# Kernel optimization log

Hardware: AMD Instinct MI355X
Metric: run time of the kernel (lower is better)

The kernel has to match this reference:

```python
import jax, jax.numpy as jnp
import numpy as np
from jax import lax

EPS = 1e-5
B, T, H, L, K = 64, 1024, 12, 120, 5  # batch, seq len, hidden, lstm layers, conv kernel


def _init(key, shape, scale):
    return scale * jax.random.normal(key, shape, dtype=jnp.float32)


def setup_inputs() -> dict:
    key = jax.random.key(0)
    ks = jax.random.split(key, 16)
    return {
        "x": jax.random.normal(ks[0], (B, 6, T), dtype=jnp.float32),
        "conv_acc_w": _init(ks[1], (6, 6, K), 0.3),
        "conv_acc_b": jnp.zeros((6,), jnp.float32),
        "bn1_gamma": jnp.ones((6,), jnp.float32),
        "bn1_beta": jnp.zeros((6,), jnp.float32),
        "conv_ang_w": _init(ks[2], (6, 6, K), 0.3),
        "conv_ang_b": jnp.zeros((6,), jnp.float32),
        "bn2_gamma": jnp.ones((6,), jnp.float32),
        "bn2_beta": jnp.zeros((6,), jnp.float32),
        "attn_w": _init(ks[3], (H, 6), 0.4),
        "attn_b": jnp.zeros((H,), jnp.float32),
        "lstm_wih": _init(ks[4], (L, 4 * H, H), 0.2),
        "lstm_whh": _init(ks[5], (L, 4 * H, H), 0.2),
        "lstm_bih": _init(ks[6], (L, 4 * H), 0.1),
        "lstm_bhh": _init(ks[7], (L, 4 * H), 0.1),
        "lin1_w": _init(ks[8], (H, H), 0.3),
        "lin1_b": jnp.zeros((H,), jnp.float32),
        "lin2_w": _init(ks[9], (H, H), 0.3),
        "lin2_b": jnp.zeros((H,), jnp.float32),
        "mu_w": _init(ks[10], (H, H), 0.3),
        "mu_b": jnp.zeros((H,), jnp.float32),
        "sigma_w": _init(ks[11], (H, H), 0.3),
        "sigma_b": jnp.zeros((H,), jnp.float32),
    }


def _conv1d(x, w, b):
    # x: (B, C, T) valid conv, matches nn.Conv1d
    y = lax.conv_general_dilated(x, w, (1,), "VALID", dimension_numbers=("NCH", "OIH", "NCH"))
    return y + b[None, :, None]


def _batchnorm(x, gamma, beta):
    # training-mode BatchNorm1d: biased batch stats over (N, T)
    mean = jnp.mean(x, axis=(0, 2), keepdims=True)
    var = jnp.var(x, axis=(0, 2), keepdims=True)
    return (x - mean) * lax.rsqrt(var + EPS) * gamma[None, :, None] + beta[None, :, None]


def _lstm_stack(seq_tbh, wih, whh, bias):
    # seq_tbh: (T', B, H); stacked 120-layer LSTM, torch gate order (i, f, g, o)
    b = seq_tbh.shape[1]
    h0 = jnp.zeros((b, H), seq_tbh.dtype)

    def layer(seq, p):
        w_ih, w_hh, bb = p

        def step(carry, xt):
            h, c = carry
            g = xt @ w_ih.T + h @ w_hh.T + bb  # (B, 4H)
            i, f, gg, o = jnp.split(g, 4, axis=-1)
            c_new = jax.nn.sigmoid(f) * c + jax.nn.sigmoid(i) * jnp.tanh(gg)
            h_new = jax.nn.sigmoid(o) * jnp.tanh(c_new)
            return (h_new, c_new), h_new

        (h_T, _), out = lax.scan(step, (h0, h0), seq)
        return out, h_T

    _, h_last = lax.scan(layer, seq_tbh, (wih, whh, bias))
    return h_last  # (L, B, H): final hidden state of every layer


def _forward(x, conv_acc_w, conv_acc_b, bn1_gamma, bn1_beta, conv_ang_w, conv_ang_b,
             bn2_gamma, bn2_beta, attn_w, attn_b, lstm_wih, lstm_whh, lstm_bih, lstm_bhh,
             lin1_w, lin1_b, lin2_w, lin2_b, mu_w, mu_b, sigma_w, sigma_b):
    out_acc = jax.nn.relu(_batchnorm(_conv1d(x, conv_acc_w, conv_acc_b), bn1_gamma, bn1_beta))
    out_ang = jax.nn.relu(_batchnorm(_conv1d(out_acc, conv_ang_w, conv_ang_b), bn2_gamma, bn2_beta))
    feat = jax.nn.relu(jnp.einsum("bct,hc->bth", out_ang, attn_w) + attn_b)  # (B, T-8, H)
    seq = jnp.transpose(feat, (1, 0, 2))  # (T', B, H) time-major for scan
    h_last = _lstm_stack(seq, lstm_wih, lstm_whh, lstm_bih + lstm_bhh)
    h = jnp.transpose(h_last, (1, 0, 2))  # (B, L, H) == hidden_state.permute(1,0,2)
    h = jax.nn.relu(h @ lin1_w.T + lin1_b)
    out = jax.nn.relu(h @ lin2_w.T + lin2_b)
    mu = out @ mu_w.T + mu_b
    log_var = jax.nn.softplus(out @ sigma_w.T + sigma_b)
    return out, mu, log_var


def reference(x, conv_acc_w, conv_acc_b, bn1_gamma, bn1_beta, conv_ang_w, conv_ang_b,
              bn2_gamma, bn2_beta, attn_w, attn_b, lstm_wih, lstm_whh, lstm_bih, lstm_bhh,
              lin1_w, lin1_b, lin2_w, lin2_b, mu_w, mu_b, sigma_w, sigma_b):
    return _forward(x, conv_acc_w, conv_acc_b, bn1_gamma, bn1_beta, conv_ang_w, conv_ang_b,
                    bn2_gamma, bn2_beta, attn_w, attn_b, lstm_wih, lstm_whh, lstm_bih, lstm_bhh,
                    lin1_w, lin1_b, lin2_w, lin2_b, mu_w, mu_b, sigma_w, sigma_b)
```

## Files before the change

kernel.cpp:

```cpp
#include <hip/hip_runtime.h>
#include <math.h>

#define NLAY 120
#define TT   1016
#define NB   64
#define RB   8
#define IRS  32
#define TPB  384
#define BIGF (1 << 20)

typedef float v2f __attribute__((ext_vector_type(2)));

__device__ __forceinline__ float fast_rcp(float x) { return __builtin_amdgcn_rcpf(x); }
__device__ __forceinline__ float fast_sig(float x) { return fast_rcp(1.f + __expf(-x)); }
__device__ __forceinline__ float fast_tanh(float x) { return 1.f - 2.f * fast_rcp(1.f + __expf(2.f * x)); }

__device__ __forceinline__ int poll_ge_ag(const int* p, int tgt, int cur) {
  long g = 0;
  while (cur < tgt) {
    cur = __hip_atomic_load(p, __ATOMIC_RELAXED, __HIP_MEMORY_SCOPE_AGENT);
    if (++g > 2000000L) break;
  }
  return cur;
}
__device__ __forceinline__ int poll_ge_wg(const int* p, int tgt, int cur) {
  long g = 0;
  while (cur < tgt) {
    cur = __hip_atomic_load(p, __ATOMIC_RELAXED, __HIP_MEMORY_SCOPE_WORKGROUP);
    if (++g > 2000000L) break;
  }
  return cur;
}

__global__ void k_conv(const float* __restrict__ xin, const float* __restrict__ cw,
                       const float* __restrict__ cb, const float* __restrict__ aff,
                       float* __restrict__ yout, float* __restrict__ stat,
                       int Tin, int Tout, int use_aff)
{
  const int bx = blockIdx.x;
  const int b = bx / 6, co = bx - b * 6;
  const int tid = threadIdx.x;
  __shared__ float wsh[30];
  __shared__ float ssh[6], shsh[6];
  if (tid < 30) wsh[tid] = cw[co * 30 + tid];
  if (tid < 6) {
    ssh[tid]  = use_aff ? aff[tid] : 1.f;
    shsh[tid] = use_aff ? aff[6 + tid] : 0.f;
  }
  __syncthreads();
  const float bias = cb[co];
  float lsum = 0.f, lsq = 0.f;
  for (int t = tid; t < Tout; t += 256) {
    float acc = bias;
#pragma unroll
    for (int ci = 0; ci < 6; ++ci) {
      const float* xr = xin + ((size_t)b * 6 + ci) * Tin + t;
      const float s = ssh[ci], sh = shsh[ci];
#pragma unroll
      for (int k = 0; k < 5; ++k) {
        float v = xr[k];
        if (use_aff) v = fmaxf(fmaf(s, v, sh), 0.f);
        acc += wsh[ci * 5 + k] * v;
      }
    }
    yout[((size_t)b * 6 + co) * Tout + t] = acc;
    lsum += acc; lsq += acc * acc;
  }
  __shared__ float rs[256], rq[256];
  rs[tid] = lsum; rq[tid] = lsq;
  __syncthreads();
  for (int s = 128; s > 0; s >>= 1) {
    if (tid < s) { rs[tid] += rs[tid + s]; rq[tid] += rq[tid + s]; }
    __syncthreads();
  }
  if (tid == 0) { atomicAdd(&stat[co], rs[0]); atomicAdd(&stat[6 + co], rq[0]); }
}

__global__ void k_finalize(const float* __restrict__ stat,
                           const float* __restrict__ gamma, const float* __restrict__ beta,
                           float* __restrict__ aff, float invN)
{
  const int c = threadIdx.x;
  if (c < 6) {
    float mean = stat[c] * invN;
    float var  = stat[6 + c] * invN - mean * mean;
    float sc   = gamma[c] * rsqrtf(var + 1e-5f);
    aff[c]     = sc;
    aff[6 + c] = fmaf(-mean, sc, beta[c]);
  }
}

__global__ void k_attn(const float* __restrict__ y2, const float* __restrict__ aff2,
                       const float* __restrict__ aw, const float* __restrict__ ab,
                       float* __restrict__ seq0)
{
  const int t = blockIdx.x;
  const int tid = threadIdx.x;
  __shared__ float zb[6 * 64];
  if (tid < 384) {
    const int c = tid >> 6, bb = tid & 63;
    float v = y2[((size_t)bb * 6 + c) * TT + t];
    zb[c * 64 + bb] = fmaxf(fmaf(aff2[c], v, aff2[6 + c]), 0.f);
  }
  __syncthreads();
  const int b = tid / 12, j = tid - b * 12;
  float acc = ab[j];
#pragma unroll
  for (int c = 0; c < 6; ++c) acc += aw[j * 6 + c] * zb[c * 64 + b];
  seq0[(size_t)t * 768 + tid] = fmaxf(acc, 0.f);
}

__global__ __launch_bounds__(TPB, 2) void k_lstm(
    const float* __restrict__ wih, const float* __restrict__ whh,
    const float* __restrict__ bih, const float* __restrict__ bhh,
    const float* __restrict__ seq0, float* __restrict__ ring,
    int* __restrict__ prog, int* __restrict__ cons,
    float* __restrict__ hfin)
{
  const int bid  = blockIdx.x;
  const int c    = bid >> 2;
  const int seg  = bid & 3;
  const int tid  = threadIdx.x;
  const int w    = tid >> 6;
  const int lane = tid & 63;
  const int p    = lane / 12;
  const int j    = lane - p * 12;
  const bool act = (p < 5);
  const int pc   = act ? p : 0;
  const int l    = seg * 30 + w * 5 + pc;

  __shared__ __align__(16) float hloc[6][2][60];
  __shared__ __align__(16) float iring[5][IRS][12];
  __shared__ __align__(16) float xring[2][16][12];
  __shared__ __align__(16) float oring[16][12];
  __shared__ int pflag[6];
  __shared__ int cflag[8];
  float* xrf = &xring[0][0][0];

  if (tid < 6) pflag[tid] = 0;
  if (tid < 8) cflag[tid] = 0;
  if (lane < 60) { hloc[w][0][lane] = 0.f; hloc[w][1][lane] = 0.f; }
  __syncthreads();

  v2f wx_if[12], wx_go[12], wh_if[12], wh_go[12];
  v2f b_if = (v2f){0.f, 0.f}, b_go = (v2f){0.f, 0.f};
  if (act) {
    const float* wi = wih + l * 576;
    const float* wh = whh + l * 576;
#pragma unroll
    for (int k = 0; k < 12; ++k) {
      wx_if[k] = (v2f){ wi[(j     ) * 12 + k], wi[(j + 12) * 12 + k] };
      wx_go[k] = (v2f){ wi[(j + 24) * 12 + k], wi[(j + 36) * 12 + k] };
      wh_if[k] = (v2f){ wh[(j     ) * 12 + k], wh[(j + 12) * 12 + k] };
      wh_go[k] = (v2f){ wh[(j + 24) * 12 + k], wh[(j + 36) * 12 + k] };
    }
    const float* ba = bih + l * 48;
    const float* bb = bhh + l * 48;
    b_if = (v2f){ ba[j]      + bb[j],      ba[j + 12] + bb[j + 12] };
    b_go = (v2f){ ba[j + 24] + bb[j + 24], ba[j + 36] + bb[j + 36] };
  }

  const int hop_in  = c * 3 + seg - 1;
  const int hop_out = c * 3 + seg;
  const float* rin  = ring + (size_t)((seg > 0) ? hop_in : 0) * (RB * 192);
  float*       rout = ring + (size_t)((seg < 3) ? hop_out : 0) * (RB * 192);
  const bool is_feeder = (w == 0);
  const bool is_tailer = (w == 5) && (seg < 3);

  const int f0 = lane, f1 = lane + 64, f2 = lane + 128;
  const int s0o0 = (f0 / 12) * 768 + (f0 % 12);
  const int s0o1 = (f1 / 12) * 768 + (f1 % 12);
  const int s0o2 = (f2 / 12) * 768 + (f2 % 12);

  auto ld_batch = [&](int m, float* d) {
    if (seg == 0) {
      const float* b = seq0 + (size_t)m * 16 * 768 + c * 12;
      d[0] = b[s0o0]; d[1] = b[s0o1]; d[2] = b[s0o2];
    } else {
      const float* b = rin + (m & (RB - 1)) * 192;
      d[0] = __hip_atomic_load(b + f0, __ATOMIC_RELAXED, __HIP_MEMORY_SCOPE_AGENT);
      d[1] = __hip_atomic_load(b + f1, __ATOMIC_RELAXED, __HIP_MEMORY_SCOPE_AGENT);
      d[2] = __hip_atomic_load(b + f2, __ATOMIC_RELAXED, __HIP_MEMORY_SCOPE_AGENT);
    }
  };

  float pend[3] = {0.f, 0.f, 0.f};
  int kp = 0, kcons = 0;
  if (is_feeder) {
    if (seg > 0) kp = poll_ge_ag(&prog[hop_in], 2, 0);
    float cur[3];
    ld_batch(0, cur);
    ld_batch(1, pend);
    xrf[f0] = cur[0]; xrf[f1] = cur[1]; xrf[f2] = cur[2];
  }

  float cst = 0.f;
  int pcache = 0, ccache = 0;

  for (int m = 0; m < NB; ++m) {
    if (is_feeder) {
      if (m + 1 < NB) {
        float* xd = xrf + ((m + 1) & 1) * 192;
        xd[f0] = pend[0]; xd[f1] = pend[1]; xd[f2] = pend[2];
      }
      if (m + 2 < NB) {
        if (seg > 0 && kp < m + 3) kp = poll_ge_ag(&prog[hop_in], m + 3, kp);
        ld_batch(m + 2, pend);
      }
      if (seg > 0 && lane == 0)
        __hip_atomic_store(&cons[hop_in], m, __ATOMIC_RELAXED, __HIP_MEMORY_SCOPE_AGENT);
    }

#pragma unroll
    for (int u = 0; u < 16; ++u) {
      const int s = m * 16 + u;

      if ((u & 3) == 0) {
        if (w > 0 && s < TT) {
          int tgt = (s + 4 < TT) ? (s + 4) : TT;
          if (pcache < tgt) {
            pcache = poll_ge_wg(&pflag[w - 1], tgt, pcache);
            __builtin_amdgcn_fence(__ATOMIC_ACQUIRE, "workgroup");
          }
        }
        if (w < 5 && s >= 33) {
          int tgt = s - 32;
          if (ccache < tgt) ccache = poll_ge_wg(&cflag[w + 1], tgt, ccache);
        }
      }

      const int t  = s - pc;
      const bool run = act && (t >= 0) && (t < TT);
      const int rb = (s & 1) ^ 1, wb = s & 1;

      const float* ax;
      if (p == 0) ax = (w == 0) ? (xrf + ((s >> 4) & 1) * 192 + (s & 15) * 12)
                                : (&iring[w - 1][s & (IRS - 1)][0]);
      else        ax = &hloc[w][rb][(pc == 0 ? 0 : pc - 1) * 12];
      const float* ah = &hloc[w][rb][pc * 12];

      float4 xA = ((const float4*)ax)[0], xB = ((const float4*)ax)[1], xC = ((const float4*)ax)[2];
      float4 hA = ((const float4*)ah)[0], hB = ((const float4*)ah)[1], hC = ((const float4*)ah)[2];
      float xv[12] = {xA.x,xA.y,xA.z,xA.w, xB.x,xB.y,xB.z,xB.w, xC.x,xC.y,xC.z,xC.w};
      float hv[12] = {hA.x,hA.y,hA.z,hA.w, hB.x,hB.y,hB.z,hB.w, hC.x,hC.y,hC.z,hC.w};

      v2f axif = (v2f){0.f,0.f}, axgo = (v2f){0.f,0.f};
      v2f ahif = b_if, ahgo = b_go;
#pragma unroll
      for (int k = 0; k < 12; ++k) {
        v2f xx = { xv[k], xv[k] };
        axif = __builtin_elementwise_fma(wx_if[k], xx, axif);
        axgo = __builtin_elementwise_fma(wx_go[k], xx, axgo);
      }
#pragma unroll
      for (int k = 0; k < 12; ++k) {
        v2f hh = { hv[k], hv[k] };
        ahif = __builtin_elementwise_fma(wh_if[k], hh, ahif);
        ahgo = __builtin_elementwise_fma(wh_go[k], hh, ahgo);
      }
      v2f aif = axif + ahif, ago = axgo + ahgo;
      float ig = fast_sig(aif.x);
      float fg = fast_sig(aif.y);
      float gg = fast_tanh(ago.x);
      float og = fast_sig(ago.y);

      if (run) {
        cst = fg * cst + ig * gg;
        float hn = og * fast_tanh(cst);
        hloc[w][wb][p * 12 + j] = hn;
        if (p == 4) {
          if (w < 5) iring[w][t & (IRS - 1)][j] = hn;
          else if (seg < 3) oring[t & 15][j] = hn;
        }
        if (t == TT - 1) hfin[l * 768 + c * 12 + j] = hn;
      }

      if (is_tailer) {
        const int t4 = s - 4;
        if (t4 >= 0 && t4 < TT && (((t4 & 15) == 15) || t4 == TT - 1)) {
          const int m4 = t4 >> 4;
          if (kcons < m4 - (RB - 1) + 1)
            kcons = poll_ge_ag(&cons[hop_out], m4 - RB + 1, kcons);
          const float* orf = &oring[0][0];
          float o0 = orf[f0], o1 = orf[f1], o2 = orf[f2];
          float* d = rout + (m4 & (RB - 1)) * 192;
          __hip_atomic_store(d + f0, o0, __ATOMIC_RELAXED, __HIP_MEMORY_SCOPE_AGENT);
          __hip_atomic_store(d + f1, o1, __ATOMIC_RELAXED, __HIP_MEMORY_SCOPE_AGENT);
          __hip_atomic_store(d + f2, o2, __ATOMIC_RELAXED, __HIP_MEMORY_SCOPE_AGENT);
          if (lane == 0)
            __hip_atomic_store(&prog[hop_out], m4 + 1, __ATOMIC_RELEASE, __HIP_MEMORY_SCOPE_AGENT);
        }
      }

      if ((u & 3) == 3 && lane == 0) {
        if (w < 5)
          __hip_atomic_store(&pflag[w], s - 3, __ATOMIC_RELEASE, __HIP_MEMORY_SCOPE_WORKGROUP);
        if (w > 0)
          __hip_atomic_store(&cflag[w], s + 1, __ATOMIC_RELEASE, __HIP_MEMORY_SCOPE_WORKGROUP);
      }
    }
  }

  if (lane == 0) {
    if (w < 5) __hip_atomic_store(&pflag[w], BIGF, __ATOMIC_RELEASE, __HIP_MEMORY_SCOPE_WORKGROUP);
    if (w > 0) __hip_atomic_store(&cflag[w], BIGF, __ATOMIC_RELEASE, __HIP_MEMORY_SCOPE_WORKGROUP);
    if (is_feeder && seg > 0)
      __hip_atomic_store(&cons[hop_in], BIGF, __ATOMIC_RELAXED, __HIP_MEMORY_SCOPE_AGENT);
  }
}

__global__ void k_head(const float* __restrict__ hfin,
                       const float* __restrict__ w1, const float* __restrict__ b1,
                       const float* __restrict__ w2, const float* __restrict__ b2,
                       const float* __restrict__ wm, const float* __restrict__ bm,
                       const float* __restrict__ wsg, const float* __restrict__ bsg,
                       float* __restrict__ out)
{
  const int tid = threadIdx.x;
  __shared__ float s1[144], s2[144], sm[144], ss[144];
  __shared__ float v1[12], v2[12], vm[12], vs[12];
  if (tid < 144) { s1[tid] = w1[tid]; s2[tid] = w2[tid]; sm[tid] = wm[tid]; ss[tid] = wsg[tid]; }
  if (tid < 12)  { v1[tid] = b1[tid]; v2[tid] = b2[tid]; vm[tid] = bm[tid]; vs[tid] = bsg[tid]; }
  __syncthreads();
  const int r = blockIdx.x * 256 + tid;
  const int b = r / 120, l = r - b * 120;
  float h[12];
#pragma unroll
  for (int k = 0; k < 12; ++k) h[k] = hfin[l * 768 + b * 12 + k];
  float u1[12];
#pragma unroll
  for (int u = 0; u < 12; ++u) {
    float a = v1[u];
#pragma unroll
    for (int k = 0; k < 12; ++k) a += s1[u * 12 + k] * h[k];
    u1[u] = fmaxf(a, 0.f);
  }
  float u2[12];
#pragma unroll
  for (int u = 0; u < 12; ++u) {
    float a = v2[u];
#pragma unroll
    for (int k = 0; k < 12; ++k) a += s2[u * 12 + k] * u1[k];
    u2[u] = fmaxf(a, 0.f);
  }
  const size_t base = (size_t)r * 12;
#pragma unroll
  for (int u = 0; u < 12; ++u) out[base + u] = u2[u];
#pragma unroll
  for (int u = 0; u < 12; ++u) {
    float a = vm[u];
#pragma unroll
    for (int k = 0; k < 12; ++k) a += sm[u * 12 + k] * u2[k];
    out[92160 + base + u] = a;
  }
#pragma unroll
  for (int u = 0; u < 12; ++u) {
    float a = vs[u];
#pragma unroll
    for (int k = 0; k < 12; ++k) a += ss[u * 12 + k] * u2[k];
    out[184320 + base + u] = fmaxf(a, 0.f) + log1pf(expf(-fabsf(a)));
  }
}

extern "C" void kernel_launch(void* const* d_in, const int* in_sizes, int n_in,
                              void* d_out, int out_size, void* d_ws, size_t ws_size,
                              hipStream_t stream)
{
  const float* x   = (const float*)d_in[0];
  const float* c1w = (const float*)d_in[1];
  const float* c1b = (const float*)d_in[2];
  const float* g1  = (const float*)d_in[3];
  const float* be1 = (const float*)d_in[4];
  const float* c2w = (const float*)d_in[5];
  const float* c2b = (const float*)d_in[6];
  const float* g2  = (const float*)d_in[7];
  const float* be2 = (const float*)d_in[8];
  const float* aw  = (const float*)d_in[9];
  const float* ab  = (const float*)d_in[10];
  const float* wih = (const float*)d_in[11];
  const float* whh = (const float*)d_in[12];
  const float* bih = (const float*)d_in[13];
  const float* bhh = (const float*)d_in[14];
  const float* l1w = (const float*)d_in[15];
  const float* l1b = (const float*)d_in[16];
  const float* l2w = (const float*)d_in[17];
  const float* l2b = (const float*)d_in[18];
  const float* muw = (const float*)d_in[19];
  const float* mub = (const float*)d_in[20];
  const float* sgw = (const float*)d_in[21];
  const float* sgb = (const float*)d_in[22];

  float* ws    = (float*)d_ws;
  float* stat1 = ws;
  float* stat2 = ws + 12;
  float* aff1  = ws + 24;
  float* aff2  = ws + 36;
  int*   prog  = (int*)(ws + 64);
  int*   cons  = (int*)(ws + 304);
  float* y1    = ws + 576;
  float* y2    = y1 + 391680;
  float* seq0  = y2 + 390144;
  float* ring  = seq0 + 780288;
  float* hfin  = ring + (size_t)192 * RB * 192;

  hipMemsetAsync(d_ws, 0, 576 * sizeof(float), stream);

  k_conv<<<384, 256, 0, stream>>>(x, c1w, c1b, nullptr, y1, stat1, 1024, 1020, 0);
  k_finalize<<<1, 64, 0, stream>>>(stat1, g1, be1, aff1, 1.f / 65280.f);
  k_conv<<<384, 256, 0, stream>>>(y1, c2w, c2b, aff1, y2, stat2, 1020, 1016, 1);
  k_finalize<<<1, 64, 0, stream>>>(stat2, g2, be2, aff2, 1.f / 65024.f);
  k_attn<<<1016, 768, 0, stream>>>(y2, aff2, aw, ab, seq0);
  k_lstm<<<256, TPB, 0, stream>>>(wih, whh, bih, bhh, seq0, ring, prog, cons, hfin);
  k_head<<<30, 256, 0, stream>>>(hfin, l1w, l1b, l2w, l2b, muw, mub, sgw, sgb, (float*)d_out);
}
```

Before: 856.6 us.

## Restructure LSTM wavefront loop with relaxed intra-block flags and unguarded steady-state steps

Replaces the 64x16 nested loop with a flat loop over groups of four steps. Steps in the steady-state range skip the per-step bounds checks and final-output write. Intra-workgroup flags switch from release/acquire atomics and fences to relaxed stores and loads with compiler-only barriers, and spin loops add s_sleep with a lower iteration cap. The goal is less synchronisation and branch overhead on the latency-bound recurrence. It risks memory-ordering bugs between wavefronts, because only compiler barriers remain, and extra wake-up latency from sleeping.

```diff
diff --git a/kernel.cpp b/kernel.cpp
--- a/kernel.cpp
+++ b/kernel.cpp
@@ -19,7 +19,9 @@
   long g = 0;
   while (cur < tgt) {
     cur = __hip_atomic_load(p, __ATOMIC_RELAXED, __HIP_MEMORY_SCOPE_AGENT);
-    if (++g > 2000000L) break;
+    if (cur >= tgt) break;
+    __builtin_amdgcn_s_sleep(1);
+    if (++g > 400000L) break;
   }
   return cur;
 }
@@ -27,7 +29,9 @@
   long g = 0;
   while (cur < tgt) {
     cur = __hip_atomic_load(p, __ATOMIC_RELAXED, __HIP_MEMORY_SCOPE_WORKGROUP);
-    if (++g > 2000000L) break;
+    if (cur >= tgt) break;
+    __builtin_amdgcn_s_sleep(1);
+    if (++g > 400000L) break;
   }
   return cur;
 }
@@ -129,7 +133,7 @@
   const int pc   = act ? p : 0;
   const int l    = seg * 30 + w * 5 + pc;
 
-  __shared__ __align__(16) float hloc[6][2][60];
+  __shared__ __align__(16) float hloc[6][2][64];
   __shared__ __align__(16) float iring[5][IRS][12];
   __shared__ __align__(16) float xring[2][16][12];
   __shared__ __align__(16) float oring[16][12];
@@ -139,7 +143,7 @@
 
   if (tid < 6) pflag[tid] = 0;
   if (tid < 8) cflag[tid] = 0;
-  if (lane < 60) { hloc[w][0][lane] = 0.f; hloc[w][1][lane] = 0.f; }
+  hloc[w][0][lane] = 0.f; hloc[w][1][lane] = 0.f;
   __syncthreads();
 
   v2f wx_if[12], wx_go[12], wh_if[12], wh_go[12];
@@ -197,73 +201,51 @@
   float cst = 0.f;
   int pcache = 0, ccache = 0;
 
-  for (int m = 0; m < NB; ++m) {
-    if (is_feeder) {
-      if (m + 1 < NB) {
-        float* xd = xrf + ((m + 1) & 1) * 192;
-        xd[f0] = pend[0]; xd[f1] = pend[1]; xd[f2] = pend[2];
-      }
-      if (m + 2 < NB) {
-        if (seg > 0 && kp < m + 3) kp = poll_ge_ag(&prog[hop_in], m + 3, kp);
-        ld_batch(m + 2, pend);
-      }
-      if (seg > 0 && lane == 0)
-        __hip_atomic_store(&cons[hop_in], m, __ATOMIC_RELAXED, __HIP_MEMORY_SCOPE_AGENT);
-    }
-
-#pragma unroll
-    for (int u = 0; u < 16; ++u) {
-      const int s = m * 16 + u;
-
-      if ((u & 3) == 0) {
-        if (w > 0 && s < TT) {
-          int tgt = (s + 4 < TT) ? (s + 4) : TT;
-          if (pcache < tgt) {
-            pcache = poll_ge_wg(&pflag[w - 1], tgt, pcache);
-            __builtin_amdgcn_fence(__ATOMIC_ACQUIRE, "workgroup");
-          }
-        }
-        if (w < 5 && s >= 33) {
-          int tgt = s - 32;
-          if (ccache < tgt) ccache = poll_ge_wg(&cflag[w + 1], tgt, ccache);
-        }
-      }
-
-      const int t  = s - pc;
+  auto step = [&](int s, bool guard) __attribute__((always_inline)) {
+    const int t  = s - pc;
+    const int rb = (s & 1) ^ 1, wb = s & 1;
+
+    const float* ax;
+    if (p == 0) ax = (w == 0) ? (xrf + ((s >> 4) & 1) * 192 + (s & 15) * 12)
+                              : (&iring[w - 1][s & (IRS - 1)][0]);
+    else        ax = &hloc[w][rb][(pc == 0 ? 0 : pc - 1) * 12];
+    const float* ah = &hloc[w][rb][pc * 12];
+
+    float4 xA = ((const float4*)ax)[0], xB = ((const float4*)ax)[1], xC = ((const float4*)ax)[2];
+    float4 hA = ((const float4*)ah)[0], hB = ((const float4*)ah)[1], hC = ((const float4*)ah)[2];
+    float xv[12] = {xA.x,xA.y,xA.z,xA.w, xB.x,xB.y,xB.z,xB.w, xC.x,xC.y,xC.z,xC.w};
+    float hv[12] = {hA.x,hA.y,hA.z,hA.w, hB.x,hB.y,hB.z,hB.w, hC.x,hC.y,hC.z,hC.w};
+
+    v2f axif = (v2f){0.f,0.f}, axgo = (v2f){0.f,0.f};
+    v2f ahif = b_if, ahgo = b_go;
+#pragma unroll
+    for (int k = 0; k < 12; ++k) {
+      v2f xx = { xv[k], xv[k] };
+      axif = __builtin_elementwise_fma(wx_if[k], xx, axif);
+      axgo = __builtin_elementwise_fma(wx_go[k], xx, axgo);
+    }
+#pragma unroll
+    for (int k = 0; k < 12; ++k) {
+      v2f hh = { hv[k], hv[k] };
+      ahif = __builtin_elementwise_fma(wh_if[k], hh, ahif);
+      ahgo = __builtin_elementwise_fma(wh_go[k], hh, ahgo);
+    }
+    v2f aif = axif + ahif, ago = axgo + ahgo;
+    float ig = fast_sig(aif.x);
+    float fg = fast_sig(aif.y);
+    float gg = fast_tanh(ago.x);
+    float og = fast_sig(ago.y);
+
+    if (!guard) {
+      cst = fg * cst + ig * gg;
+      float hn = og * fast_tanh(cst);
+      hloc[w][wb][p * 12 + j] = hn;
+      if (p == 4) {
+        if (w < 5) iring[w][t & (IRS - 1)][j] = hn;
+        else if (seg < 3) oring[t & 15][j] = hn;
+      }
+    } else {
       const bool run = act && (t >= 0) && (t < TT);
-      const int rb = (s & 1) ^ 1, wb = s & 1;
-
-      const float* ax;
-      if (p == 0) ax = (w == 0) ? (xrf + ((s >> 4) & 1) * 192 + (s & 15) * 12)
-                                : (&iring[w - 1][s & (IRS - 1)][0]);
-      else        ax = &hloc[w][rb][(pc == 0 ? 0 : pc - 1) * 12];
-      const float* ah = &hloc[w][rb][pc * 12];
-
-      float4 xA = ((const float4*)ax)[0], xB = ((const float4*)ax)[1], xC = ((const float4*)ax)[2];
-      float4 hA = ((const float4*)ah)[0], hB = ((const float4*)ah)[1], hC = ((const float4*)ah)[2];
-      float xv[12] = {xA.x,xA.y,xA.z,xA.w, xB.x,xB.y,xB.z,xB.w, xC.x,xC.y,xC.z,xC.w};
-      float hv[12] = {hA.x,hA.y,hA.z,hA.w, hB.x,hB.y,hB.z,hB.w, hC.x,hC.y,hC.z,hC.w};
-
-      v2f axif = (v2f){0.f,0.f}, axgo = (v2f){0.f,0.f};
-      v2f ahif = b_if, ahgo = b_go;
-#pragma unroll
-      for (int k = 0; k < 12; ++k) {
-        v2f xx = { xv[k], xv[k] };
-        axif = __builtin_elementwise_fma(wx_if[k], xx, axif);
-        axgo = __builtin_elementwise_fma(wx_go[k], xx, axgo);
-      }
-#pragma unroll
-      for (int k = 0; k < 12; ++k) {
-        v2f hh = { hv[k], hv[k] };
-        ahif = __builtin_elementwise_fma(wh_if[k], hh, ahif);
-        ahgo = __builtin_elementwise_fma(wh_go[k], hh, ahgo);
-      }
-      v2f aif = axif + ahif, ago = axgo + ahgo;
-      float ig = fast_sig(aif.x);
-      float fg = fast_sig(aif.y);
-      float gg = fast_tanh(ago.x);
-      float og = fast_sig(ago.y);
-
       if (run) {
         cst = fg * cst + ig * gg;
         float hn = og * fast_tanh(cst);
@@ -274,36 +256,75 @@
         }
         if (t == TT - 1) hfin[l * 768 + c * 12 + j] = hn;
       }
-
-      if (is_tailer) {
-        const int t4 = s - 4;
-        if (t4 >= 0 && t4 < TT && (((t4 & 15) == 15) || t4 == TT - 1)) {
-          const int m4 = t4 >> 4;
-          if (kcons < m4 - (RB - 1) + 1)
-            kcons = poll_ge_ag(&cons[hop_out], m4 - RB + 1, kcons);
-          const float* orf = &oring[0][0];
-          float o0 = orf[f0], o1 = orf[f1], o2 = orf[f2];
-          float* d = rout + (m4 & (RB - 1)) * 192;
-          __hip_atomic_store(d + f0, o0, __ATOMIC_RELAXED, __HIP_MEMORY_SCOPE_AGENT);
-          __hip_atomic_store(d + f1, o1, __ATOMIC_RELAXED, __HIP_MEMORY_SCOPE_AGENT);
-          __hip_atomic_store(d + f2, o2, __ATOMIC_RELAXED, __HIP_MEMORY_SCOPE_AGENT);
-          if (lane == 0)
-            __hip_atomic_store(&prog[hop_out], m4 + 1, __ATOMIC_RELEASE, __HIP_MEMORY_SCOPE_AGENT);
-        }
-      }
-
-      if ((u & 3) == 3 && lane == 0) {
-        if (w < 5)
-          __hip_atomic_store(&pflag[w], s - 3, __ATOMIC_RELEASE, __HIP_MEMORY_SCOPE_WORKGROUP);
-        if (w > 0)
-          __hip_atomic_store(&cflag[w], s + 1, __ATOMIC_RELEASE, __HIP_MEMORY_SCOPE_WORKGROUP);
-      }
+    }
+
+    if (is_tailer) {
+      const int t4 = s - 4;
+      if (t4 >= 0 && t4 < TT && (((t4 & 15) == 15) || t4 == TT - 1)) {
+        const int m4 = t4 >> 4;
+        if (kcons < m4 - (RB - 1) + 1)
+          kcons = poll_ge_ag(&cons[hop_out], m4 - RB + 1, kcons);
+        const float* orf = &oring[0][0];
+        float o0 = orf[f0], o1 = orf[f1], o2 = orf[f2];
+        float* d = rout + (m4 & (RB - 1)) * 192;
+        __hip_atomic_store(d + f0, o0, __ATOMIC_RELAXED, __HIP_MEMORY_SCOPE_AGENT);
+        __hip_atomic_store(d + f1, o1, __ATOMIC_RELAXED, __HIP_MEMORY_SCOPE_AGENT);
+        __hip_atomic_store(d + f2, o2, __ATOMIC_RELAXED, __HIP_MEMORY_SCOPE_AGENT);
+        if (lane == 0)
+          __hip_atomic_store(&prog[hop_out], m4 + 1, __ATOMIC_RELEASE, __HIP_MEMORY_SCOPE_AGENT);
+      }
+    }
+  };
+
+  for (int s4 = 0; s4 < 1024; s4 += 4) {
+    if (is_feeder && (s4 & 15) == 0) {
+      const int m = s4 >> 4;
+      if (m + 1 < NB) {
+        float* xd = xrf + ((m + 1) & 1) * 192;
+        xd[f0] = pend[0]; xd[f1] = pend[1]; xd[f2] = pend[2];
+      }
+      if (m + 2 < NB) {
+        if (seg > 0 && kp < m + 3) kp = poll_ge_ag(&prog[hop_in], m + 3, kp);
+        ld_batch(m + 2, pend);
+      }
+      if (seg > 0 && lane == 0)
+        __hip_atomic_store(&cons[hop_in], m, __ATOMIC_RELAXED, __HIP_MEMORY_SCOPE_AGENT);
+    }
+
+    if (w > 0 && s4 < TT) {
+      const int tgt = (s4 + 4 < TT) ? (s4 + 4) : TT;
+      if (pcache < tgt) {
+        pcache = poll_ge_wg(&pflag[w - 1], tgt, pcache);
+        asm volatile("" ::: "memory");
+      }
+    }
+    if (w < 5 && s4 >= 36) {
+      const int tgt = s4 - 32;
+      if (ccache < tgt) {
+        ccache = poll_ge_wg(&cflag[w + 1], tgt, ccache);
+        asm volatile("" ::: "memory");
+      }
+    }
+
+    if (s4 >= 4 && s4 < 1012) {
+      step(s4 + 0, false); step(s4 + 1, false); step(s4 + 2, false); step(s4 + 3, false);
+    } else {
+      step(s4 + 0, true);  step(s4 + 1, true);  step(s4 + 2, true);  step(s4 + 3, true);
+    }
+
+    if (lane == 0) {
+      asm volatile("" ::: "memory");
+      if (w < 5)
+        __hip_atomic_store(&pflag[w], s4, __ATOMIC_RELAXED, __HIP_MEMORY_SCOPE_WORKGROUP);
+      if (w > 0 && s4 + 3 < TT)
+        __hip_atomic_store(&cflag[w], s4 + 4, __ATOMIC_RELAXED, __HIP_MEMORY_SCOPE_WORKGROUP);
     }
   }
 
   if (lane == 0) {
-    if (w < 5) __hip_atomic_store(&pflag[w], BIGF, __ATOMIC_RELEASE, __HIP_MEMORY_SCOPE_WORKGROUP);
-    if (w > 0) __hip_atomic_store(&cflag[w], BIGF, __ATOMIC_RELEASE, __HIP_MEMORY_SCOPE_WORKGROUP);
+    asm volatile("" ::: "memory");
+    if (w < 5) __hip_atomic_store(&pflag[w], BIGF, __ATOMIC_RELAXED, __HIP_MEMORY_SCOPE_WORKGROUP);
+    if (w > 0) __hip_atomic_store(&cflag[w], BIGF, __ATOMIC_RELAXED, __HIP_MEMORY_SCOPE_WORKGROUP);
     if (is_feeder && seg > 0)
       __hip_atomic_store(&cons[hop_in], BIGF, __ATOMIC_RELAXED, __HIP_MEMORY_SCOPE_AGENT);
   }
```

Result: faster. 811.2 us (-5.3%).
